# Performance work log

Measured on AMD Instinct MI355X. Metric: run time of the kernel, lower is better.

Reference implementation:

```python
import jax, jax.numpy as jnp
import numpy as np

NUM_USERS = 100000
NUM_ITEMS = 200000
N = NUM_USERS + NUM_ITEMS
D = 64
NNZ = 5_000_000
B = 16384
N_LAYERS = 3


def setup_inputs() -> dict:
    key = jax.random.key(0)
    ks = jax.random.split(key, 7)
    users = jax.random.randint(ks[0], (B,), 0, NUM_USERS, dtype=jnp.int32)
    items = jax.random.randint(ks[1], (B,), 0, NUM_ITEMS, dtype=jnp.int32)
    edge_row = jax.random.randint(ks[2], (NNZ,), 0, N, dtype=jnp.int32)
    edge_col = jax.random.randint(ks[3], (NNZ,), 0, N, dtype=jnp.int32)
    # mimic D^-1/2 A D^-1/2 normalization scale (~1/avg_degree)
    edge_vals = jax.random.uniform(ks[4], (NNZ,), dtype=jnp.float32) * 0.06
    user_emb = jax.random.normal(ks[5], (NUM_USERS, D), dtype=jnp.float32) * 0.1
    item_emb = jax.random.normal(ks[6], (NUM_ITEMS, D), dtype=jnp.float32) * 0.1
    return {
        "users": users, "items": items,
        "edge_row": edge_row, "edge_col": edge_col, "edge_vals": edge_vals,
        "user_emb": user_emb, "item_emb": item_emb,
        "n_layers": N_LAYERS,
    }


def _spmm(edge_row, edge_col, edge_vals, x):
    # sparse [N,N] @ dense [N,D] via gather + segment_sum
    msg = x[edge_col] * edge_vals[:, None]  # [nnz, D]
    return jax.ops.segment_sum(msg, edge_row, num_segments=N)


def reference(users, items, edge_row, edge_col, edge_vals, user_emb, item_emb, n_layers):
    # LightGCN.computer(): propagate + mean over layers (running-sum form)
    all_emb = jnp.concatenate([user_emb, item_emb], axis=0)  # [N, D]
    acc = all_emb
    for _ in range(n_layers):
        all_emb = _spmm(edge_row, edge_col, edge_vals, all_emb)
        acc = acc + all_emb
    light_out = acc / (n_layers + 1)
    all_users = light_out[:NUM_USERS]
    all_items = light_out[NUM_USERS:]
    # forward(users, items): elementwise dot product
    users_emb = all_users[users]
    items_emb = all_items[items]
    gamma = jnp.sum(users_emb * items_emb, axis=1)  # [B]
    return gamma
```

## Files before the change

### kernel.cpp

```cpp
#include <hip/hip_runtime.h>
#include <hip/hip_fp16.h>
#include <hip/hip_fp8.h>

namespace {

constexpr int kUsers = 100000;
constexpr int kItems = 200000;
constexpr int kN     = kUsers + kItems;
constexpr int kD     = 64;
constexpr int kNNZ   = 5000000;
constexpr int kB     = 16384;
constexpr int kRowsPerBkt = 2048;
constexpr int kNBKT  = (kN + kRowsPerBkt - 1) / kRowsPerBkt;
constexpr int kSEPB  = 4096;
constexpr int kCE    = 8192;
constexpr int kMC    = 5;
constexpr int kCap   = kMC * kCE;
constexpr int kMaxSub = 2 * kB;

typedef int   v2i __attribute__((ext_vector_type(2)));
typedef float v4f __attribute__((ext_vector_type(4)));


__device__ inline void dec4(unsigned int w, float& f0, float& f1, float& f2, float& f3) {
  unsigned int a = ((w & 0x007f007fu) << 7) | ((w & 0x00800080u) << 8);
  unsigned int b = (((w >> 8) & 0x007f007fu) << 7) | (((w >> 8) & 0x00800080u) << 8);
  float2 e = __half22float2(*reinterpret_cast<const __half2*>(&a));
  float2 o = __half22float2(*reinterpret_cast<const __half2*>(&b));
  f0 = e.x; f1 = o.x; f2 = e.y; f3 = o.y;
}

__device__ inline float dec1x4(unsigned char b) {
  unsigned int hb = ((b & 0x7fu) << 7) | ((b & 0x80u) << 8);
  return __half2float(__ushort_as_half((unsigned short)hb)) * 4.0f;
}

__device__ inline unsigned char enc(float f) { __hip_fp8_e4m3 q(f); return q.__x; }

__global__ void zero_i32(int* __restrict__ p, int n) {
  int i = blockIdx.x * blockDim.x + threadIdx.x;
  if (i < n) p[i] = 0;
}

__global__ void bucket_scatter(const int* __restrict__ row, const int* __restrict__ col,
                               const float* __restrict__ val, int* __restrict__ gpos,
                               int2* __restrict__ tmp) {
  __shared__ int hcnt[4][kNBKT];
  __shared__ int lofs[kNBKT];
  __shared__ int hbase[kNBKT];
  __shared__ int lds[256];
  __shared__ int2 se[kSEPB];
  __shared__ unsigned short sb[kSEPB];
  int t = threadIdx.x;
  int wv = t >> 6;
  long base = (long)blockIdx.x * kSEPB;
  int valid = (int)min((long)kSEPB, (long)kNNZ - base);
  for (int i = t; i < kNBKT; i += 256) {
    hcnt[0][i] = 0; hcnt[1][i] = 0; hcnt[2][i] = 0; hcnt[3][i] = 0;
  }
  __syncthreads();
  int pk[16], bk[16], rk[16];
  float v[16];
  bool ok[16];
#pragma unroll
  for (int j = 0; j < 16; ++j) {
    long i = base + j * 256 + t;
    ok[j] = (i < kNNZ);
    if (ok[j]) {
      int r = __builtin_nontemporal_load(row + i);
      bk[j] = r >> 11;
      pk[j] = ((r & 2047) << 19) | __builtin_nontemporal_load(col + i);
      v[j] = __builtin_nontemporal_load(val + i);
      rk[j] = atomicAdd(&hcnt[wv][bk[j]], 1);
    }
  }
  __syncthreads();
  int own = 0;
  if (t < kNBKT) {
    int c0 = hcnt[0][t], c1 = hcnt[1][t], c2 = hcnt[2][t], c3 = hcnt[3][t];
    hcnt[0][t] = 0; hcnt[1][t] = c0; hcnt[2][t] = c0 + c1; hcnt[3][t] = c0 + c1 + c2;
    own = c0 + c1 + c2 + c3;
  }
  lds[t] = own;
  __syncthreads();
  for (int o = 1; o < 256; o <<= 1) {
    int x = (t >= o) ? lds[t - o] : 0;
    __syncthreads();
    if (t >= o) lds[t] += x;
    __syncthreads();
  }
  if (t < kNBKT) {
    lofs[t] = lds[t] - own;
    hbase[t] = t * kCap + atomicAdd(&gpos[t], own);
  }
  __syncthreads();
#pragma unroll
  for (int j = 0; j < 16; ++j) {
    if (ok[j]) {
      int pos = lofs[bk[j]] + hcnt[wv][bk[j]] + rk[j];
      se[pos] = make_int2(pk[j], __float_as_int(v[j]));
      sb[pos] = (unsigned short)bk[j];
    }
  }
  __syncthreads();
#pragma unroll
  for (int j = 0; j < 16; ++j) {
    int pos = t + j * 256;
    if (pos < valid) {
      int b = sb[pos];
      tmp[hbase[b] + (pos - lofs[b])] = se[pos];
    }
  }
}

__global__ void chunk_hist(const int* __restrict__ gpos, const int2* __restrict__ tmp,
                           int* __restrict__ ctab) {
  __shared__ int h[kRowsPerBkt];
  int b = blockIdx.x / kMC, c = blockIdx.x % kMC;
  int t = threadIdx.x;
  for (int i = t; i < kRowsPerBkt; i += 256) h[i] = 0;
  __syncthreads();
  int s = b * kCap + c * kCE;
  int e = b * kCap + gpos[b];
  if (s + kCE < e) e = s + kCE;
  for (int j = s + t; j < e; j += 256) atomicAdd(&h[tmp[j].x >> 19], 1);
  __syncthreads();
  int* dst = ctab + (size_t)blockIdx.x * kRowsPerBkt;
  for (int i = t; i < kRowsPerBkt; i += 256) dst[i] = h[i];
}

__global__ void scanA(int* __restrict__ ctab, int* __restrict__ rowptr,
                      int* __restrict__ partials) {
  __shared__ int lsum[256];
  int b = blockIdx.x, t = threadIdx.x;
  int cnt[8];
#pragma unroll
  for (int k = 0; k < 8; ++k) cnt[k] = 0;
  for (int c = 0; c < kMC; ++c) {
    int* p = ctab + (size_t)(b * kMC + c) * kRowsPerBkt;
#pragma unroll
    for (int k = 0; k < 8; ++k) {
      int idx = t * 8 + k;
      int v = p[idx];
      p[idx] = cnt[k];
      cnt[k] += v;
    }
  }
  int s = 0, pref[8];
#pragma unroll
  for (int k = 0; k < 8; ++k) { pref[k] = s; s += cnt[k]; }
  lsum[t] = s;
  __syncthreads();
  for (int o = 1; o < 256; o <<= 1) {
    int v = (t >= o) ? lsum[t - o] : 0;
    __syncthreads();
    if (t >= o) lsum[t] += v;
    __syncthreads();
  }
  int ex = (t == 0) ? 0 : lsum[t - 1];
#pragma unroll
  for (int k = 0; k < 8; ++k) {
    int r = b * kRowsPerBkt + t * 8 + k;
    if (r < kN) rowptr[r] = ex + pref[k];
  }
  if (t == 255) partials[b] = lsum[255];
}

__global__ void scan2(int* __restrict__ partials) {
  __shared__ int lds[256];
  int t = threadIdx.x;
  lds[t] = (t < kNBKT) ? partials[t] : 0;
  __syncthreads();
  for (int o = 1; o < 256; o <<= 1) {
    int v = (t >= o) ? lds[t - o] : 0;
    __syncthreads();
    if (t >= o) lds[t] += v;
    __syncthreads();
  }
  int ex = (t == 0) ? 0 : lds[t - 1];
  if (t < kNBKT) partials[t] = ex;
}

__global__ void scan3(int* __restrict__ rowptr, const int* __restrict__ partials) {
  int i = blockIdx.x * blockDim.x + threadIdx.x;
  if (i < kN) rowptr[i] += partials[i >> 11];
  else if (i == kN) rowptr[kN] = kNNZ;
}

__global__ void chunk_place(const int* __restrict__ gpos, const int2* __restrict__ tmp,
                            const int* __restrict__ rowptr, const int* __restrict__ ctab,
                            int2* __restrict__ edges) {
  __shared__ int rank[kRowsPerBkt];
  int b = blockIdx.x / kMC, c = blockIdx.x % kMC;
  int t = threadIdx.x;
  for (int i = t; i < kRowsPerBkt; i += 256) rank[i] = 0;
  __syncthreads();
  int s = b * kCap + c * kCE;
  int e = b * kCap + gpos[b];
  if (s + kCE < e) e = s + kCE;
  const int* coff = ctab + (size_t)blockIdx.x * kRowsPerBkt;
  for (int j = s + t; j < e; j += 256) {
    int2 epk = tmp[j];
    int rl = epk.x >> 19;
    int k = atomicAdd(&rank[rl], 1);
    int dst = rowptr[b * kRowsPerBkt + rl] + coff[rl] + k;
    edges[dst] = make_int2(epk.x & 0x7FFFF, epk.y);
  }
}

__global__ void mark_rows(const int* __restrict__ users, const int* __restrict__ items,
                          int* __restrict__ mark) {
  int i = blockIdx.x * blockDim.x + threadIdx.x;
  if (i >= kB) return;
  mark[users[i]] = 1;
  mark[kUsers + items[i]] = 1;
}

__global__ void sub_hist(const int* __restrict__ rowptr, const int* __restrict__ mark,
                         int* __restrict__ dh) {
  __shared__ int h[64];
  int t = threadIdx.x;
  if (t < 64) h[t] = 0;
  __syncthreads();
  int i = blockIdx.x * 256 + t;
  if (i < kN && mark[i]) {
    int d = min(rowptr[i + 1] - rowptr[i], 63);
    atomicAdd(&h[d], 1);
  }
  __syncthreads();
  if (t < 64 && h[t]) atomicAdd(&dh[t], h[t]);
}

__global__ void deg_scan(int* __restrict__ dh, int* __restrict__ scnt) {
  int t = threadIdx.x;
  int v = dh[t];
  int x = v;
  for (int o = 1; o < 64; o <<= 1) {
    int y = __shfl_up(x, o, 64);
    if (t >= o) x += y;
  }
  if (t == 63) *scnt = x;
  dh[t] = x - v;
}

__global__ void sub_place(const int* __restrict__ rowptr, const int* __restrict__ mark,
                          int* __restrict__ dh, int* __restrict__ list) {
  __shared__ int h[64], base[64];
  int t = threadIdx.x;
  if (t < 64) h[t] = 0;
  __syncthreads();
  int i = blockIdx.x * 256 + t;
  int d = 0, lr = 0;
  bool okv = (i < kN) && mark[i];
  if (okv) {
    d = min(rowptr[i + 1] - rowptr[i], 63);
    lr = atomicAdd(&h[d], 1);
  }
  __syncthreads();
  if (t < 64) base[t] = h[t] ? atomicAdd(&dh[t], h[t]) : 0;
  __syncthreads();
  if (okv) list[base[d] + lr] = i;
}

__global__ void to_fp8(const float* __restrict__ ue, const float* __restrict__ ie,
                       unsigned char* __restrict__ xq) {
  int t = blockIdx.x * blockDim.x + threadIdx.x;
  if (t >= kN * kD / 8) return;
  int row = t >> 3;
  int seg = t & 7;
  const float* src = (row < kUsers) ? (ue + (size_t)row * kD + seg * 8)
                                    : (ie + (size_t)(row - kUsers) * kD + seg * 8);
  v4f a = __builtin_nontemporal_load((const v4f*)src);
  v4f b = __builtin_nontemporal_load((const v4f*)src + 1);
  float f[8] = {a.x, a.y, a.z, a.w, b.x, b.y, b.z, b.w};
  unsigned int w0 = 0, w1 = 0;
#pragma unroll
  for (int k = 0; k < 4; ++k) w0 |= (unsigned int)enc(f[k] * 64.f) << (8 * k);
#pragma unroll
  for (int k = 0; k < 4; ++k) w1 |= (unsigned int)enc(f[4 + k] * 64.f) << (8 * k);
  v2i o; o.x = (int)w0; o.y = (int)w1;
  ((v2i*)xq)[t] = o;
}

template <bool SUBSET>
__global__ __launch_bounds__(256, 8) void spmm(
    const int* __restrict__ rowptr, const int2* __restrict__ edges,
    const unsigned char* __restrict__ x, unsigned char* __restrict__ yq,
    const int* __restrict__ list, const int* __restrict__ cnt) {
  int t = threadIdx.x;
  int l = t & 7;
  int wid = (blockIdx.x * 256 + t) >> 6;
  int g = (t >> 3) & 7;
  int p = wid * 8 + g;
  int r = -1;
  if (SUBSET) {
    int n = *cnt;
    if (p < n) r = list[p];
  } else {
    if (p < kN) r = p;
  }
  int s = 0, e = 0;
  if (r >= 0) { s = rowptr[r]; e = rowptr[r + 1]; }
  int mx = e - s;
#pragma unroll
  for (int m = 8; m <= 32; m <<= 1) mx = max(mx, __shfl_xor(mx, m, 64));
  float acc[8];
#pragma unroll
  for (int k = 0; k < 8; ++k) acc[k] = 0.f;
  int last = max(e - 1, 0);
  int j = s;
  int2 E0 = edges[min(j, last)];
  int2 E1 = edges[min(j + 1, last)];
  int2 E2 = edges[min(j + 2, last)];
  int2 E3 = edges[min(j + 3, last)];
  for (int it = 0; it < mx; it += 4) {
    float v0 = (j     < e) ? __int_as_float(E0.y) * 256.f : 0.f;
    float v1 = (j + 1 < e) ? __int_as_float(E1.y) * 256.f : 0.f;
    float v2 = (j + 2 < e) ? __int_as_float(E2.y) * 256.f : 0.f;
    float v3 = (j + 3 < e) ? __int_as_float(E3.y) * 256.f : 0.f;
    v2i h0 = ((const v2i*)(x + (size_t)E0.x * kD))[l];
    v2i h1 = ((const v2i*)(x + (size_t)E1.x * kD))[l];
    v2i h2 = ((const v2i*)(x + (size_t)E2.x * kD))[l];
    v2i h3 = ((const v2i*)(x + (size_t)E3.x * kD))[l];
    j += 4;
    E0 = edges[min(j, last)];
    E1 = edges[min(j + 1, last)];
    E2 = edges[min(j + 2, last)];
    E3 = edges[min(j + 3, last)];
    float f0, f1, f2, f3;
    dec4((unsigned int)h0.x, f0, f1, f2, f3);
    acc[0] = fmaf(v0, f0, acc[0]); acc[1] = fmaf(v0, f1, acc[1]);
    acc[2] = fmaf(v0, f2, acc[2]); acc[3] = fmaf(v0, f3, acc[3]);
    dec4((unsigned int)h0.y, f0, f1, f2, f3);
    acc[4] = fmaf(v0, f0, acc[4]); acc[5] = fmaf(v0, f1, acc[5]);
    acc[6] = fmaf(v0, f2, acc[6]); acc[7] = fmaf(v0, f3, acc[7]);
    dec4((unsigned int)h1.x, f0, f1, f2, f3);
    acc[0] = fmaf(v1, f0, acc[0]); acc[1] = fmaf(v1, f1, acc[1]);
    acc[2] = fmaf(v1, f2, acc[2]); acc[3] = fmaf(v1, f3, acc[3]);
    dec4((unsigned int)h1.y, f0, f1, f2, f3);
    acc[4] = fmaf(v1, f0, acc[4]); acc[5] = fmaf(v1, f1, acc[5]);
    acc[6] = fmaf(v1, f2, acc[6]); acc[7] = fmaf(v1, f3, acc[7]);
    dec4((unsigned int)h2.x, f0, f1, f2, f3);
    acc[0] = fmaf(v2, f0, acc[0]); acc[1] = fmaf(v2, f1, acc[1]);
    acc[2] = fmaf(v2, f2, acc[2]); acc[3] = fmaf(v2, f3, acc[3]);
    dec4((unsigned int)h2.y, f0, f1, f2, f3);
    acc[4] = fmaf(v2, f0, acc[4]); acc[5] = fmaf(v2, f1, acc[5]);
    acc[6] = fmaf(v2, f2, acc[6]); acc[7] = fmaf(v2, f3, acc[7]);
    dec4((unsigned int)h3.x, f0, f1, f2, f3);
    acc[0] = fmaf(v3, f0, acc[0]); acc[1] = fmaf(v3, f1, acc[1]);
    acc[2] = fmaf(v3, f2, acc[2]); acc[3] = fmaf(v3, f3, acc[3]);
    dec4((unsigned int)h3.y, f0, f1, f2, f3);
    acc[4] = fmaf(v3, f0, acc[4]); acc[5] = fmaf(v3, f1, acc[5]);
    acc[6] = fmaf(v3, f2, acc[6]); acc[7] = fmaf(v3, f3, acc[7]);
  }
  if (r >= 0) {
    unsigned int w0 = 0, w1 = 0;
#pragma unroll
    for (int k = 0; k < 4; ++k) w0 |= (unsigned int)enc(acc[k]) << (8 * k);
#pragma unroll
    for (int k = 0; k < 4; ++k) w1 |= (unsigned int)enc(acc[4 + k]) << (8 * k);
    v2i o; o.x = (int)w0; o.y = (int)w1;
    ((v2i*)yq)[(size_t)r * 8 + l] = o;
  }
}

__global__ void acc_add_init(const int* __restrict__ users, const int* __restrict__ items,
                             const float* __restrict__ uemb, const float* __restrict__ iemb,
                             const unsigned char* __restrict__ xq, float* __restrict__ uacc,
                             float* __restrict__ iacc) {
  int tid = blockIdx.x * blockDim.x + threadIdx.x;
  if (tid >= kB * kD) return;
  int b = tid >> 6, d = tid & 63;
  int u = users[b], iw = items[b];
  uacc[tid] = uemb[(size_t)u * kD + d] + dec1x4(xq[(size_t)u * kD + d]);
  iacc[tid] = iemb[(size_t)iw * kD + d] + dec1x4(xq[(size_t)(kUsers + iw) * kD + d]);
}

__global__ void acc_add(const int* __restrict__ users, const int* __restrict__ items,
                        const unsigned char* __restrict__ xq, float* __restrict__ uacc,
                        float* __restrict__ iacc) {
  int tid = blockIdx.x * blockDim.x + threadIdx.x;
  if (tid >= kB * kD) return;
  int b = tid >> 6, d = tid & 63;
  uacc[tid] += dec1x4(xq[(size_t)users[b] * kD + d]);
  iacc[tid] += dec1x4(xq[(size_t)(kUsers + items[b]) * kD + d]);
}

__global__ void acc_add_fin(const int* __restrict__ users, const int* __restrict__ items,
                            const unsigned char* __restrict__ xq, const float* __restrict__ uacc,
                            const float* __restrict__ iacc, float* __restrict__ out) {
  int tid = blockIdx.x * blockDim.x + threadIdx.x;
  if (tid >= kB * kD) return;
  int b = tid >> 6, d = tid & 63;
  float u = uacc[tid] + dec1x4(xq[(size_t)users[b] * kD + d]);
  float v = iacc[tid] + dec1x4(xq[(size_t)(kUsers + items[b]) * kD + d]);
  float p = u * v;
  for (int o = 32; o > 0; o >>= 1) p += __shfl_down(p, o, 64);
  if (d == 0) out[b] = p * 0.0625f;
}

}

extern "C" void kernel_launch(void* const* d_in, const int* in_sizes, int n_in,
                              void* d_out, int out_size, void* d_ws, size_t ws_size,
                              hipStream_t stream) {
  const int*   users = (const int*)d_in[0];
  const int*   items = (const int*)d_in[1];
  const int*   erow  = (const int*)d_in[2];
  const int*   ecol  = (const int*)d_in[3];
  const float* evals = (const float*)d_in[4];
  const float* uemb  = (const float*)d_in[5];
  const float* iemb  = (const float*)d_in[6];
  float* out = (float*)d_out;

  char* ws = (char*)d_ws;
  size_t off = 0;
  auto take = [&](size_t bytes) -> char* {
    char* p = ws + off;
    off = (off + bytes + 255) & ~(size_t)255;
    return p;
  };
  int*    rowptr   = (int*)take((size_t)(kN + 1) * 4);
  int*    gpos     = (int*)take((kNBKT + 1) * 4);
  int*    partials = (int*)take(256 * 4);
  int*    mark     = (int*)take((size_t)kN * 4);
  int*    list     = (int*)take((size_t)kMaxSub * 4);
  int*    scnt     = (int*)take(256);
  int2*   edges    = (int2*)take((size_t)kNNZ * 8);
  int2*   tmp      = (int2*)take((size_t)kNBKT * kCap * 8);
  unsigned char* xq0 = (unsigned char*)take((size_t)kN * kD);
  unsigned char* xq1 = (unsigned char*)take((size_t)kN * kD);
  float*  uacc     = (float*)take((size_t)kB * kD * 4);
  float*  iacc     = (float*)take((size_t)kB * kD * 4);
  int*    ctab     = (int*)xq0;
  int*    dh       = partials;
  (void)ws_size; (void)in_sizes; (void)n_in; (void)out_size;

  const int nScatBlocks = (kNNZ + kSEPB - 1) / kSEPB;
  const int nSpmmBlocks = (kN + 31) / 32;
  const int nSubBlocks  = (kMaxSub + 31) / 32;
  const int nRowBlocks  = (kN + 255) / 256;

  zero_i32<<<1, 256, 0, stream>>>(gpos, kNBKT + 1);
  zero_i32<<<nRowBlocks, 256, 0, stream>>>(mark, kN);
  bucket_scatter<<<nScatBlocks, 256, 0, stream>>>(erow, ecol, evals, gpos, tmp);
  chunk_hist<<<kNBKT * kMC, 256, 0, stream>>>(gpos, tmp, ctab);
  scanA<<<kNBKT, 256, 0, stream>>>(ctab, rowptr, partials);
  scan2<<<1, 256, 0, stream>>>(partials);
  scan3<<<(kN + 1 + 255) / 256, 256, 0, stream>>>(rowptr, partials);
  chunk_place<<<kNBKT * kMC, 256, 0, stream>>>(gpos, tmp, rowptr, ctab, edges);

  mark_rows<<<(kB + 255) / 256, 256, 0, stream>>>(users, items, mark);
  zero_i32<<<1, 64, 0, stream>>>(dh, 64);
  sub_hist<<<nRowBlocks, 256, 0, stream>>>(rowptr, mark, dh);
  deg_scan<<<1, 64, 0, stream>>>(dh, scnt);
  sub_place<<<nRowBlocks, 256, 0, stream>>>(rowptr, mark, dh, list);

  to_fp8<<<(kN * kD / 8 + 255) / 256, 256, 0, stream>>>(uemb, iemb, xq0);
  spmm<false><<<nSpmmBlocks, 256, 0, stream>>>(rowptr, edges, xq0, xq1, nullptr, nullptr);
  acc_add_init<<<(kB * kD) / 256, 256, 0, stream>>>(users, items, uemb, iemb, xq1, uacc, iacc);
  spmm<false><<<nSpmmBlocks, 256, 0, stream>>>(rowptr, edges, xq1, xq0, nullptr, nullptr);
  acc_add<<<(kB * kD) / 256, 256, 0, stream>>>(users, items, xq0, uacc, iacc);
  spmm<true ><<<nSubBlocks, 256, 0, stream>>>(rowptr, edges, xq0, xq1, list, scnt);
  acc_add_fin<<<(kB * kD) / 256, 256, 0, stream>>>(users, items, xq1, uacc, iacc, out);
}
```

Before: 543.4 us.

## Pack edges into 32-bit words, prune layer-2 rows, use native fp8 decode

Edges become a single 32-bit word holding the 19-bit column and a 13-bit truncated half-precision value, which halves edge storage and the bandwidth spent reading edges in every SpMM layer. A new mark_cols pass marks the neighbours of the rows needed in the final layer, and the second SpMM computes only those marked rows instead of all N. The fp8 decode uses native conversion builtins when available, and the zero-fill launches are merged into one kernel. The trade-offs are lower precision on the edge weights, an extra serial per-row loop in mark_cols, and branch divergence in the second SpMM.

```diff
diff --git a/kernel.cpp b/kernel.cpp
--- a/kernel.cpp
+++ b/kernel.cpp
@@ -21,25 +21,61 @@
 typedef int   v2i __attribute__((ext_vector_type(2)));
 typedef float v4f __attribute__((ext_vector_type(4)));
 
-
-__device__ inline void dec4(unsigned int w, float& f0, float& f1, float& f2, float& f3) {
-  unsigned int a = ((w & 0x007f007fu) << 7) | ((w & 0x00800080u) << 8);
-  unsigned int b = (((w >> 8) & 0x007f007fu) << 7) | (((w >> 8) & 0x00800080u) << 8);
-  float2 e = __half22float2(*reinterpret_cast<const __half2*>(&a));
-  float2 o = __half22float2(*reinterpret_cast<const __half2*>(&b));
-  f0 = e.x; f1 = o.x; f2 = e.y; f3 = o.y;
-}
-
-__device__ inline float dec1x4(unsigned char b) {
+#if defined(__has_builtin)
+#if __has_builtin(__builtin_amdgcn_cvt_pk_f32_fp8) && __has_builtin(__builtin_amdgcn_cvt_f32_fp8)
+#define NATIVE_FP8 1
+#endif
+#endif
+#ifndef NATIVE_FP8
+#define NATIVE_FP8 0
+#endif
+
+constexpr float kValScale = NATIVE_FP8 ? 1.0f : 256.0f;
+
+__device__ inline void dec8(v2i h, float* f) {
+#if NATIVE_FP8
+  auto a0 = __builtin_amdgcn_cvt_pk_f32_fp8(h.x, false);
+  auto a1 = __builtin_amdgcn_cvt_pk_f32_fp8(h.x, true);
+  auto a2 = __builtin_amdgcn_cvt_pk_f32_fp8(h.y, false);
+  auto a3 = __builtin_amdgcn_cvt_pk_f32_fp8(h.y, true);
+  f[0] = a0[0]; f[1] = a0[1]; f[2] = a1[0]; f[3] = a1[1];
+  f[4] = a2[0]; f[5] = a2[1]; f[6] = a3[0]; f[7] = a3[1];
+#else
+  unsigned int ws[2] = {(unsigned int)h.x, (unsigned int)h.y};
+#pragma unroll
+  for (int q = 0; q < 2; ++q) {
+    unsigned int w = ws[q];
+    unsigned int a = ((w & 0x007f007fu) << 7) | ((w & 0x00800080u) << 8);
+    unsigned int b = (((w >> 8) & 0x007f007fu) << 7) | (((w >> 8) & 0x00800080u) << 8);
+    float2 e = __half22float2(*reinterpret_cast<const __half2*>(&a));
+    float2 o = __half22float2(*reinterpret_cast<const __half2*>(&b));
+    f[4 * q + 0] = e.x; f[4 * q + 1] = o.x; f[4 * q + 2] = e.y; f[4 * q + 3] = o.y;
+  }
+#endif
+}
+
+__device__ inline float dec1(unsigned char b) {
+#if NATIVE_FP8
+  return __builtin_amdgcn_cvt_f32_fp8((int)b, 0) * 0.015625f;
+#else
   unsigned int hb = ((b & 0x7fu) << 7) | ((b & 0x80u) << 8);
   return __half2float(__ushort_as_half((unsigned short)hb)) * 4.0f;
+#endif
 }
 
 __device__ inline unsigned char enc(float f) { __hip_fp8_e4m3 q(f); return q.__x; }
 
-__global__ void zero_i32(int* __restrict__ p, int n) {
+__device__ inline float vdec(int w) {
+  return __half2float(__ushort_as_half((unsigned short)((w >> 17) & 0x7FFC))) * kValScale;
+}
+
+__global__ void zero3(int* __restrict__ gpos, int* __restrict__ mark,
+                      int* __restrict__ dh, int* __restrict__ scnt) {
   int i = blockIdx.x * blockDim.x + threadIdx.x;
-  if (i < n) p[i] = 0;
+  if (i < kN) mark[i] = 0;
+  if (i < kNBKT + 1) gpos[i] = 0;
+  if (i < 64) dh[i] = 0;
+  if (i == 0) scnt[0] = 0;
 }
 
 __global__ void bucket_scatter(const int* __restrict__ row, const int* __restrict__ col,
@@ -59,8 +95,7 @@
     hcnt[0][i] = 0; hcnt[1][i] = 0; hcnt[2][i] = 0; hcnt[3][i] = 0;
   }
   __syncthreads();
-  int pk[16], bk[16], rk[16];
-  float v[16];
+  int pk[16], py[16], bk[16], rk[16];
   bool ok[16];
 #pragma unroll
   for (int j = 0; j < 16; ++j) {
@@ -68,9 +103,13 @@
     ok[j] = (i < kNNZ);
     if (ok[j]) {
       int r = __builtin_nontemporal_load(row + i);
+      int c = __builtin_nontemporal_load(col + i);
+      float v = __builtin_nontemporal_load(val + i);
       bk[j] = r >> 11;
-      pk[j] = ((r & 2047) << 19) | __builtin_nontemporal_load(col + i);
-      v[j] = __builtin_nontemporal_load(val + i);
+      pk[j] = ((r & 2047) << 19) | c;
+      unsigned short hb = __half_as_ushort(__float2half_rn(v));
+      int v13 = ((int)hb + 2) >> 2;
+      py[j] = c | (v13 << 19);
       rk[j] = atomicAdd(&hcnt[wv][bk[j]], 1);
     }
   }
@@ -98,7 +137,7 @@
   for (int j = 0; j < 16; ++j) {
     if (ok[j]) {
       int pos = lofs[bk[j]] + hcnt[wv][bk[j]] + rk[j];
-      se[pos] = make_int2(pk[j], __float_as_int(v[j]));
+      se[pos] = make_int2(pk[j], py[j]);
       sb[pos] = (unsigned short)bk[j];
     }
   }
@@ -189,7 +228,7 @@
 
 __global__ void chunk_place(const int* __restrict__ gpos, const int2* __restrict__ tmp,
                             const int* __restrict__ rowptr, const int* __restrict__ ctab,
-                            int2* __restrict__ edges) {
+                            int* __restrict__ edges) {
   __shared__ int rank[kRowsPerBkt];
   int b = blockIdx.x / kMC, c = blockIdx.x % kMC;
   int t = threadIdx.x;
@@ -204,7 +243,7 @@
     int rl = epk.x >> 19;
     int k = atomicAdd(&rank[rl], 1);
     int dst = rowptr[b * kRowsPerBkt + rl] + coff[rl] + k;
-    edges[dst] = make_int2(epk.x & 0x7FFFF, epk.y);
+    edges[dst] = epk.y;
   }
 }
 
@@ -260,6 +299,16 @@
   if (t < 64) base[t] = h[t] ? atomicAdd(&dh[t], h[t]) : 0;
   __syncthreads();
   if (okv) list[base[d] + lr] = i;
+}
+
+__global__ void mark_cols(const int* __restrict__ list, const int* __restrict__ cnt,
+                          const int* __restrict__ rowptr, const int* __restrict__ edges,
+                          int* __restrict__ mark) {
+  int p = blockIdx.x * blockDim.x + threadIdx.x;
+  if (p >= *cnt) return;
+  int r = list[p];
+  int s = rowptr[r], e = rowptr[r + 1];
+  for (int j = s; j < e; ++j) mark[edges[j] & 0x7FFFF] = 1;
 }
 
 __global__ void to_fp8(const float* __restrict__ ue, const float* __restrict__ ie,
@@ -282,25 +331,26 @@
   ((v2i*)xq)[t] = o;
 }
 
-template <bool SUBSET>
+template <int MODE>
 __global__ __launch_bounds__(256, 8) void spmm(
-    const int* __restrict__ rowptr, const int2* __restrict__ edges,
+    const int* __restrict__ rowptr, const int* __restrict__ edges,
     const unsigned char* __restrict__ x, unsigned char* __restrict__ yq,
-    const int* __restrict__ list, const int* __restrict__ cnt) {
+    const int* __restrict__ aux, const int* __restrict__ cnt) {
   int t = threadIdx.x;
   int l = t & 7;
   int wid = (blockIdx.x * 256 + t) >> 6;
   int g = (t >> 3) & 7;
   int p = wid * 8 + g;
   int r = -1;
-  if (SUBSET) {
+  bool live = false;
+  if (MODE == 2) {
     int n = *cnt;
-    if (p < n) r = list[p];
+    if (p < n) { r = aux[p]; live = true; }
   } else {
-    if (p < kN) r = p;
+    if (p < kN) { r = p; live = (MODE == 0) || (aux[r] != 0); }
   }
   int s = 0, e = 0;
-  if (r >= 0) { s = rowptr[r]; e = rowptr[r + 1]; }
+  if (live) { s = rowptr[r]; e = rowptr[r + 1]; }
   int mx = e - s;
 #pragma unroll
   for (int m = 8; m <= 32; m <<= 1) mx = max(mx, __shfl_xor(mx, m, 64));
@@ -309,51 +359,39 @@
   for (int k = 0; k < 8; ++k) acc[k] = 0.f;
   int last = max(e - 1, 0);
   int j = s;
-  int2 E0 = edges[min(j, last)];
-  int2 E1 = edges[min(j + 1, last)];
-  int2 E2 = edges[min(j + 2, last)];
-  int2 E3 = edges[min(j + 3, last)];
+  int E0 = edges[min(j, last)];
+  int E1 = edges[min(j + 1, last)];
+  int E2 = edges[min(j + 2, last)];
+  int E3 = edges[min(j + 3, last)];
   for (int it = 0; it < mx; it += 4) {
-    float v0 = (j     < e) ? __int_as_float(E0.y) * 256.f : 0.f;
-    float v1 = (j + 1 < e) ? __int_as_float(E1.y) * 256.f : 0.f;
-    float v2 = (j + 2 < e) ? __int_as_float(E2.y) * 256.f : 0.f;
-    float v3 = (j + 3 < e) ? __int_as_float(E3.y) * 256.f : 0.f;
-    v2i h0 = ((const v2i*)(x + (size_t)E0.x * kD))[l];
-    v2i h1 = ((const v2i*)(x + (size_t)E1.x * kD))[l];
-    v2i h2 = ((const v2i*)(x + (size_t)E2.x * kD))[l];
-    v2i h3 = ((const v2i*)(x + (size_t)E3.x * kD))[l];
+    float v0 = (j     < e) ? vdec(E0) : 0.f;
+    float v1 = (j + 1 < e) ? vdec(E1) : 0.f;
+    float v2 = (j + 2 < e) ? vdec(E2) : 0.f;
+    float v3 = (j + 3 < e) ? vdec(E3) : 0.f;
+    v2i h0 = ((const v2i*)(x + (size_t)(E0 & 0x7FFFF) * kD))[l];
+    v2i h1 = ((const v2i*)(x + (size_t)(E1 & 0x7FFFF) * kD))[l];
+    v2i h2 = ((const v2i*)(x + (size_t)(E2 & 0x7FFFF) * kD))[l];
+    v2i h3 = ((const v2i*)(x + (size_t)(E3 & 0x7FFFF) * kD))[l];
     j += 4;
     E0 = edges[min(j, last)];
     E1 = edges[min(j + 1, last)];
     E2 = edges[min(j + 2, last)];
     E3 = edges[min(j + 3, last)];
-    float f0, f1, f2, f3;
-    dec4((unsigned int)h0.x, f0, f1, f2, f3);
-    acc[0] = fmaf(v0, f0, acc[0]); acc[1] = fmaf(v0, f1, acc[1]);
-    acc[2] = fmaf(v0, f2, acc[2]); acc[3] = fmaf(v0, f3, acc[3]);
-    dec4((unsigned int)h0.y, f0, f1, f2, f3);
-    acc[4] = fmaf(v0, f0, acc[4]); acc[5] = fmaf(v0, f1, acc[5]);
-    acc[6] = fmaf(v0, f2, acc[6]); acc[7] = fmaf(v0, f3, acc[7]);
-    dec4((unsigned int)h1.x, f0, f1, f2, f3);
-    acc[0] = fmaf(v1, f0, acc[0]); acc[1] = fmaf(v1, f1, acc[1]);
-    acc[2] = fmaf(v1, f2, acc[2]); acc[3] = fmaf(v1, f3, acc[3]);
-    dec4((unsigned int)h1.y, f0, f1, f2, f3);
-    acc[4] = fmaf(v1, f0, acc[4]); acc[5] = fmaf(v1, f1, acc[5]);
-    acc[6] = fmaf(v1, f2, acc[6]); acc[7] = fmaf(v1, f3, acc[7]);
-    dec4((unsigned int)h2.x, f0, f1, f2, f3);
-    acc[0] = fmaf(v2, f0, acc[0]); acc[1] = fmaf(v2, f1, acc[1]);
-    acc[2] = fmaf(v2, f2, acc[2]); acc[3] = fmaf(v2, f3, acc[3]);
-    dec4((unsigned int)h2.y, f0, f1, f2, f3);
-    acc[4] = fmaf(v2, f0, acc[4]); acc[5] = fmaf(v2, f1, acc[5]);
-    acc[6] = fmaf(v2, f2, acc[6]); acc[7] = fmaf(v2, f3, acc[7]);
-    dec4((unsigned int)h3.x, f0, f1, f2, f3);
-    acc[0] = fmaf(v3, f0, acc[0]); acc[1] = fmaf(v3, f1, acc[1]);
-    acc[2] = fmaf(v3, f2, acc[2]); acc[3] = fmaf(v3, f3, acc[3]);
-    dec4((unsigned int)h3.y, f0, f1, f2, f3);
-    acc[4] = fmaf(v3, f0, acc[4]); acc[5] = fmaf(v3, f1, acc[5]);
-    acc[6] = fmaf(v3, f2, acc[6]); acc[7] = fmaf(v3, f3, acc[7]);
-  }
-  if (r >= 0) {
+    float f[8];
+    dec8(h0, f);
+#pragma unroll
+    for (int k = 0; k < 8; ++k) acc[k] = fmaf(v0, f[k], acc[k]);
+    dec8(h1, f);
+#pragma unroll
+    for (int k = 0; k < 8; ++k) acc[k] = fmaf(v1, f[k], acc[k]);
+    dec8(h2, f);
+#pragma unroll
+    for (int k = 0; k < 8; ++k) acc[k] = fmaf(v2, f[k], acc[k]);
+    dec8(h3, f);
+#pragma unroll
+    for (int k = 0; k < 8; ++k) acc[k] = fmaf(v3, f[k], acc[k]);
+  }
+  if (live) {
     unsigned int w0 = 0, w1 = 0;
 #pragma unroll
     for (int k = 0; k < 4; ++k) w0 |= (unsigned int)enc(acc[k]) << (8 * k);
@@ -372,8 +410,8 @@
   if (tid >= kB * kD) return;
   int b = tid >> 6, d = tid & 63;
   int u = users[b], iw = items[b];
-  uacc[tid] = uemb[(size_t)u * kD + d] + dec1x4(xq[(size_t)u * kD + d]);
-  iacc[tid] = iemb[(size_t)iw * kD + d] + dec1x4(xq[(size_t)(kUsers + iw) * kD + d]);
+  uacc[tid] = uemb[(size_t)u * kD + d] + dec1(xq[(size_t)u * kD + d]);
+  iacc[tid] = iemb[(size_t)iw * kD + d] + dec1(xq[(size_t)(kUsers + iw) * kD + d]);
 }
 
 __global__ void acc_add(const int* __restrict__ users, const int* __restrict__ items,
@@ -382,8 +420,8 @@
   int tid = blockIdx.x * blockDim.x + threadIdx.x;
   if (tid >= kB * kD) return;
   int b = tid >> 6, d = tid & 63;
-  uacc[tid] += dec1x4(xq[(size_t)users[b] * kD + d]);
-  iacc[tid] += dec1x4(xq[(size_t)(kUsers + items[b]) * kD + d]);
+  uacc[tid] += dec1(xq[(size_t)users[b] * kD + d]);
+  iacc[tid] += dec1(xq[(size_t)(kUsers + items[b]) * kD + d]);
 }
 
 __global__ void acc_add_fin(const int* __restrict__ users, const int* __restrict__ items,
@@ -392,8 +430,8 @@
   int tid = blockIdx.x * blockDim.x + threadIdx.x;
   if (tid >= kB * kD) return;
   int b = tid >> 6, d = tid & 63;
-  float u = uacc[tid] + dec1x4(xq[(size_t)users[b] * kD + d]);
-  float v = iacc[tid] + dec1x4(xq[(size_t)(kUsers + items[b]) * kD + d]);
+  float u = uacc[tid] + dec1(xq[(size_t)users[b] * kD + d]);
+  float v = iacc[tid] + dec1(xq[(size_t)(kUsers + items[b]) * kD + d]);
   float p = u * v;
   for (int o = 32; o > 0; o >>= 1) p += __shfl_down(p, o, 64);
   if (d == 0) out[b] = p * 0.0625f;
@@ -423,17 +461,17 @@
   int*    rowptr   = (int*)take((size_t)(kN + 1) * 4);
   int*    gpos     = (int*)take((kNBKT + 1) * 4);
   int*    partials = (int*)take(256 * 4);
+  int*    dh       = (int*)take(256 * 4);
   int*    mark     = (int*)take((size_t)kN * 4);
   int*    list     = (int*)take((size_t)kMaxSub * 4);
   int*    scnt     = (int*)take(256);
-  int2*   edges    = (int2*)take((size_t)kNNZ * 8);
+  int*    edges    = (int*)take((size_t)kNNZ * 4);
   int2*   tmp      = (int2*)take((size_t)kNBKT * kCap * 8);
   unsigned char* xq0 = (unsigned char*)take((size_t)kN * kD);
   unsigned char* xq1 = (unsigned char*)take((size_t)kN * kD);
   float*  uacc     = (float*)take((size_t)kB * kD * 4);
   float*  iacc     = (float*)take((size_t)kB * kD * 4);
   int*    ctab     = (int*)xq0;
-  int*    dh       = partials;
   (void)ws_size; (void)in_sizes; (void)n_in; (void)out_size;
 
   const int nScatBlocks = (kNNZ + kSEPB - 1) / kSEPB;
@@ -441,8 +479,7 @@
   const int nSubBlocks  = (kMaxSub + 31) / 32;
   const int nRowBlocks  = (kN + 255) / 256;
 
-  zero_i32<<<1, 256, 0, stream>>>(gpos, kNBKT + 1);
-  zero_i32<<<nRowBlocks, 256, 0, stream>>>(mark, kN);
+  zero3<<<nRowBlocks, 256, 0, stream>>>(gpos, mark, dh, scnt);
   bucket_scatter<<<nScatBlocks, 256, 0, stream>>>(erow, ecol, evals, gpos, tmp);
   chunk_hist<<<kNBKT * kMC, 256, 0, stream>>>(gpos, tmp, ctab);
   scanA<<<kNBKT, 256, 0, stream>>>(ctab, rowptr, partials);
@@ -451,16 +488,16 @@
   chunk_place<<<kNBKT * kMC, 256, 0, stream>>>(gpos, tmp, rowptr, ctab, edges);
 
   mark_rows<<<(kB + 255) / 256, 256, 0, stream>>>(users, items, mark);
-  zero_i32<<<1, 64, 0, stream>>>(dh, 64);
   sub_hist<<<nRowBlocks, 256, 0, stream>>>(rowptr, mark, dh);
   deg_scan<<<1, 64, 0, stream>>>(dh, scnt);
   sub_place<<<nRowBlocks, 256, 0, stream>>>(rowptr, mark, dh, list);
+  mark_cols<<<(kMaxSub + 255) / 256, 256, 0, stream>>>(list, scnt, rowptr, edges, mark);
 
   to_fp8<<<(kN * kD / 8 + 255) / 256, 256, 0, stream>>>(uemb, iemb, xq0);
-  spmm<false><<<nSpmmBlocks, 256, 0, stream>>>(rowptr, edges, xq0, xq1, nullptr, nullptr);
+  spmm<0><<<nSpmmBlocks, 256, 0, stream>>>(rowptr, edges, xq0, xq1, nullptr, nullptr);
   acc_add_init<<<(kB * kD) / 256, 256, 0, stream>>>(users, items, uemb, iemb, xq1, uacc, iacc);
-  spmm<false><<<nSpmmBlocks, 256, 0, stream>>>(rowptr, edges, xq1, xq0, nullptr, nullptr);
+  spmm<1><<<nSpmmBlocks, 256, 0, stream>>>(rowptr, edges, xq1, xq0, mark, nullptr);
   acc_add<<<(kB * kD) / 256, 256, 0, stream>>>(users, items, xq0, uacc, iacc);
-  spmm<true ><<<nSubBlocks, 256, 0, stream>>>(rowptr, edges, xq0, xq1, list, scnt);
+  spmm<2><<<nSubBlocks, 256, 0, stream>>>(rowptr, edges, xq0, xq1, list, scnt);
   acc_add_fin<<<(kB * kD) / 256, 256, 0, stream>>>(users, items, xq1, uacc, iacc, out);
 }
```

New measurement: 521.5 us. 1.04x faster.
